# Kernel optimization log

Hardware: AMD Instinct MI355X
Metric: run time of the kernel (lower is better)

## Reference

```python
import jax, jax.numpy as jnp
import numpy as np

# Episode configuration (matches init_kwargs); feature map fixed by module: [64,7,7]
N_WAY, K_SHOT, Q_QUERY, PRJ = 10, 5, 100, 16
DIM, H, W = 64, 7, 7
N_SUP = N_WAY * K_SHOT * PRJ      # 800 support samples
N_QRY = N_WAY * Q_QUERY * PRJ     # 16000 query samples
B = N_SUP + N_QRY                 # 16800
TRIU_I, TRIU_J = np.triu_indices(DIM)  # row-major upper-tri indices, matches torch nonzero order


def setup_inputs() -> dict:
    key = jax.random.key(0)
    k1, k2 = jax.random.split(key)
    feat = jax.random.normal(k1, (B, DIM, H, W), dtype=jnp.float32)
    label = jax.random.randint(k2, (N_QRY,), 0, N_WAY, dtype=jnp.int64)
    # nn.Parameter init: log(1/(2*h*w)) * ones(1,1)
    temp = jnp.log(jnp.ones((1, 1), dtype=jnp.float32) / (2.0 * H * W))
    return {"feat": feat, "temp": temp, "label": label}


def _bdcovpool(x, t):
    # x: [B, dim, h, w] -> Brownian distance covariance matrix [B, dim, dim]
    b, d, h, w = x.shape
    xm = x.reshape(b, d, h * w)
    g = jnp.einsum('bim,bjm->bij', xm, xm)            # x @ x^T, [B,d,d]
    dg = jnp.diagonal(g, axis1=1, axis2=2)            # [B,d]
    # I_M @ (G*I) + (G*I) @ I_M - 2G  ==  diag_j + diag_i - 2G
    dcov = dg[:, None, :] + dg[:, :, None] - 2.0 * g
    dcov = jnp.sqrt(jnp.exp(t) * jnp.clip(dcov, 0.0) + 1e-5)
    # double centering: dcov - rowmean - colmean + totalmean
    rm = jnp.mean(dcov, axis=2, keepdims=True)        # (1/d) dcov @ I_M
    cm = jnp.mean(dcov, axis=1, keepdims=True)        # (1/d) I_M @ dcov
    tm = jnp.mean(dcov, axis=(1, 2), keepdims=True)   # (1/d^2) I_M @ dcov @ I_M
    return dcov - rm - cm + tm


def reference(feat, temp, label):
    v = _bdcovpool(feat, temp)                        # [B, 64, 64]
    tv = v[:, TRIU_I, TRIU_J]                         # Triuvec: [B, 2080]
    support = tv[:N_SUP].reshape(N_WAY, K_SHOT * PRJ, -1).mean(axis=1)  # [n_way, 2080]
    query = tv[N_SUP:]                                # [N_QRY, 2080]
    # negative squared euclidean distance (expanded form of sum((x-y)^2))
    q2 = jnp.sum(query * query, axis=1, keepdims=True)          # [N_QRY,1]
    s2 = jnp.sum(support * support, axis=1)[None, :]             # [1,n_way]
    score = -(q2 + s2 - 2.0 * jnp.einsum('nd,md->nm', query, support))  # [N_QRY, n_way]
    logp = jax.nn.log_softmax(score, axis=-1)
    loss = -jnp.mean(jnp.take_along_axis(logp, label[:, None], axis=1))
    return score, loss
```

## Files before the change

kernel.cpp:

```cpp
#include <hip/hip_runtime.h>
#include <math.h>

#define NWAY   10
#define DIMD   64
#define HWN    49
#define NSUP   800
#define NQRY   16000
#define NTRI   2080
#define FEAT_PER (DIMD*HWN)
#define LDST   68
#define KPAD   72

typedef __attribute__((ext_vector_type(8))) short bf16x8;
typedef __attribute__((ext_vector_type(4))) float f32x4;

struct __align__(16) BDCShared {
    union {
        float dcov[DIMD*LDST];
        unsigned short hl[2*DIMD*KPAD];
    } u;
    float dg[DIMD];
    float rm[DIMD];
    float psum[4*DIMD];
    float red[4*12];
    float tm;
};

__device__ __forceinline__ void k2ij(int k, int& io, int& jo) {
    int ii = (int)floorf((129.0f - sqrtf(16641.0f - 8.0f*(float)k)) * 0.5f);
    int off = ii*(129-ii)/2;
    if (off > k) { --ii; off = ii*(129-ii)/2; }
    else {
        int off2 = (ii+1)*(128-ii)/2;
        if (off2 <= k) { ii += 1; off = off2; }
    }
    io = ii;
    jo = ii + (k - off);
}

__device__ __forceinline__ unsigned short f32_to_bf16_rn(float x) {
    unsigned u = __float_as_uint(x);
    return (unsigned short)((u + 0x7fffu + ((u >> 16) & 1u)) >> 16);
}

__device__ __forceinline__ float bdc_compute(const float* __restrict__ feat,
                                             float et, int sample,
                                             BDCShared& sm) {
    const int tid = threadIdx.x;
    unsigned short* H = sm.u.hl;
    unsigned short* Lp = sm.u.hl + DIMD*KPAD;

    const float4* f4 = (const float4*)(feat + (size_t)sample * FEAT_PER);
    for (int idx = tid; idx < FEAT_PER/4; idx += 256) {
        float4 v = f4[idx];
        int e = idx * 4;
        #pragma unroll
        for (int kk = 0; kk < 4; ++kk) {
            int el = e + kk;
            int d = el / HWN;
            int m = el - d * HWN;
            float x = (&v.x)[kk];
            unsigned short hu = f32_to_bf16_rn(x);
            float hf = __uint_as_float(((unsigned)hu) << 16);
            unsigned short lu = f32_to_bf16_rn(x - hf);
            H[d*KPAD + m]  = hu;
            Lp[d*KPAD + m] = lu;
        }
    }
    for (int p = tid; p < DIMD*16; p += 256) {
        int d = p >> 4, k = 48 + (p & 15);
        if (k >= HWN) { H[d*KPAD + k] = 0; Lp[d*KPAD + k] = 0; }
    }
    __syncthreads();

    const int wv = tid >> 6, lane = tid & 63;
    const int qd = lane >> 4, c15 = lane & 15;
    const int abase = (16*wv + c15)*KPAD + qd*8;
    bf16x8 AH0 = *(const bf16x8*)&H[abase];
    bf16x8 AH1 = *(const bf16x8*)&H[abase + 32];
    bf16x8 AL0 = *(const bf16x8*)&Lp[abase];
    bf16x8 AL1 = *(const bf16x8*)&Lp[abase + 32];

    f32x4 acc[4];
    #pragma unroll
    for (int J = 0; J < 4; ++J) {
        const int bbase = (16*J + c15)*KPAD + qd*8;
        bf16x8 BH0 = *(const bf16x8*)&H[bbase];
        bf16x8 BH1 = *(const bf16x8*)&H[bbase + 32];
        bf16x8 BL0 = *(const bf16x8*)&Lp[bbase];
        bf16x8 BL1 = *(const bf16x8*)&Lp[bbase + 32];
        f32x4 a = {0.f, 0.f, 0.f, 0.f};
        a = __builtin_amdgcn_mfma_f32_16x16x32_bf16(AH0, BH0, a, 0, 0, 0);
        a = __builtin_amdgcn_mfma_f32_16x16x32_bf16(AH1, BH1, a, 0, 0, 0);
        a = __builtin_amdgcn_mfma_f32_16x16x32_bf16(AL0, BH0, a, 0, 0, 0);
        a = __builtin_amdgcn_mfma_f32_16x16x32_bf16(AL1, BH1, a, 0, 0, 0);
        a = __builtin_amdgcn_mfma_f32_16x16x32_bf16(AH0, BL0, a, 0, 0, 0);
        a = __builtin_amdgcn_mfma_f32_16x16x32_bf16(AH1, BL1, a, 0, 0, 0);
        acc[J] = a;
    }

    #pragma unroll
    for (int J = 0; J < 4; ++J) {
        if (J == wv) {
            #pragma unroll
            for (int r = 0; r < 4; ++r)
                if (c15 == 4*qd + r) sm.dg[16*wv + c15] = acc[J][r];
        }
    }
    __syncthreads();

    float* dcov = sm.u.dcov;
    float dgi[4];
    #pragma unroll
    for (int r = 0; r < 4; ++r) dgi[r] = sm.dg[16*wv + 4*qd + r];
    #pragma unroll
    for (int J = 0; J < 4; ++J) {
        int j = 16*J + c15;
        float dgj = sm.dg[j];
        #pragma unroll
        for (int r = 0; r < 4; ++r) {
            int i = 16*wv + 4*qd + r;
            float val = dgi[r] + dgj - 2.0f*acc[J][r];
            dcov[i*LDST + j] = sqrtf(et * fmaxf(val, 0.0f) + 1e-5f);
        }
    }
    __syncthreads();

    {
        int c = tid & 63, q = tid >> 6;
        float s = 0.0f;
        #pragma unroll
        for (int i2 = 0; i2 < 16; ++i2) s += dcov[(q*16 + i2)*LDST + c];
        sm.psum[q*DIMD + c] = s;
    }
    __syncthreads();
    if (tid < DIMD) {
        sm.rm[tid] = (sm.psum[tid] + sm.psum[DIMD+tid] +
                      sm.psum[2*DIMD+tid] + sm.psum[3*DIMD+tid]) * (1.0f/64.0f);
    }
    __syncthreads();
    if (tid < DIMD) {
        float v = sm.rm[tid];
        #pragma unroll
        for (int o = 32; o > 0; o >>= 1) v += __shfl_xor(v, o, 64);
        if (tid == 0) sm.tm = v * (1.0f/64.0f);
    }
    __syncthreads();
    return sm.tm;
}

__global__ void kern_init(float* __restrict__ support,
                          unsigned* __restrict__ table,
                          float* __restrict__ loss_slot) {
    int i = blockIdx.x * 256 + threadIdx.x;
    if (i < NWAY*NTRI) support[i] = 0.0f;
    if (i < NTRI) {
        int ii, jj; k2ij(i, ii, jj);
        table[i] = ((unsigned)(ii*LDST + jj) << 16) | ((unsigned)ii << 8) | (unsigned)jj;
    }
    if (i == 0) loss_slot[0] = 0.0f;
}

__global__ __launch_bounds__(256, 6) void kern_support(const float* __restrict__ feat,
                                                       const float* __restrict__ temp,
                                                       const unsigned* __restrict__ table,
                                                       float* __restrict__ support) {
    __shared__ BDCShared sm;
    float et = __expf(temp[0]);
    int s = blockIdx.x;
    float tm = bdc_compute(feat, et, s, sm);
    float* dst = support + (s / 80) * NTRI;
    for (int k = threadIdx.x; k < NTRI; k += 256) {
        unsigned t = table[k];
        float v = sm.u.dcov[t >> 16] - sm.rm[(t >> 8) & 63] - sm.rm[t & 63] + tm;
        atomicAdd(&dst[k], v * (1.0f/80.0f));
    }
}

__global__ __launch_bounds__(256) void kern_s2(const float* __restrict__ support,
                                               float* __restrict__ s2) {
    __shared__ float red[4];
    int m = blockIdx.x;
    const float* S = support + m * NTRI;
    float acc = 0.0f;
    for (int k = threadIdx.x; k < NTRI; k += 256) acc = fmaf(S[k], S[k], acc);
    int lane = threadIdx.x & 63, wv = threadIdx.x >> 6;
    #pragma unroll
    for (int o = 32; o > 0; o >>= 1) acc += __shfl_xor(acc, o, 64);
    if (lane == 0) red[wv] = acc;
    __syncthreads();
    if (threadIdx.x == 0) s2[m] = red[0] + red[1] + red[2] + red[3];
}

__global__ __launch_bounds__(256, 6) void kern_query(const float* __restrict__ feat,
                                                     const float* __restrict__ temp,
                                                     const unsigned* __restrict__ table,
                                                     const float* __restrict__ support,
                                                     const float* __restrict__ s2,
                                                     float* __restrict__ out) {
    __shared__ BDCShared sm;
    float et = __expf(temp[0]);
    int qn = blockIdx.x;
    float tm = bdc_compute(feat, et, NSUP + qn, sm);

    float qq = 0.0f;
    float cr[NWAY];
    #pragma unroll
    for (int m = 0; m < NWAY; ++m) cr[m] = 0.0f;

    for (int k = threadIdx.x; k < NTRI; k += 256) {
        unsigned t = table[k];
        float v = sm.u.dcov[t >> 16] - sm.rm[(t >> 8) & 63] - sm.rm[t & 63] + tm;
        qq = fmaf(v, v, qq);
        #pragma unroll
        for (int m = 0; m < NWAY; ++m)
            cr[m] = fmaf(v, support[m*NTRI + k], cr[m]);
    }

    int lane = threadIdx.x & 63, wv = threadIdx.x >> 6;
    #pragma unroll
    for (int m = 0; m < NWAY; ++m) {
        float v = cr[m];
        #pragma unroll
        for (int o = 32; o > 0; o >>= 1) v += __shfl_xor(v, o, 64);
        cr[m] = v;
    }
    #pragma unroll
    for (int o = 32; o > 0; o >>= 1) qq += __shfl_xor(qq, o, 64);
    if (lane == 0) {
        #pragma unroll
        for (int m = 0; m < NWAY; ++m) sm.red[wv*12 + m] = cr[m];
        sm.red[wv*12 + 10] = qq;
    }
    __syncthreads();
    if (threadIdx.x < NWAY) {
        int m = threadIdx.x;
        float CR = sm.red[m] + sm.red[12+m] + sm.red[24+m] + sm.red[36+m];
        float QQ = sm.red[10] + sm.red[22] + sm.red[34] + sm.red[46];
        out[(size_t)qn * NWAY + m] = -(QQ + s2[m] - 2.0f*CR);
    }
}

__global__ __launch_bounds__(256) void kern_loss(const float* __restrict__ score,
                                                 const int* __restrict__ label,
                                                 float* __restrict__ loss_out) {
    __shared__ float red[4];
    int n = blockIdx.x * 256 + threadIdx.x;
    float lsum = 0.0f;
    if (n < NQRY) {
        const float* srow = score + (size_t)n * NWAY;
        float s[NWAY];
        float mx = -1e30f;
        #pragma unroll
        for (int m = 0; m < NWAY; ++m) { s[m] = srow[m]; mx = fmaxf(mx, s[m]); }
        float se = 0.0f;
        #pragma unroll
        for (int m = 0; m < NWAY; ++m) se += __expf(s[m] - mx);
        float lse = mx + __logf(se);
        lsum = lse - s[label[n]];
    }
    int lane = threadIdx.x & 63, wv = threadIdx.x >> 6;
    #pragma unroll
    for (int o = 32; o > 0; o >>= 1) lsum += __shfl_xor(lsum, o, 64);
    if (lane == 0) red[wv] = lsum;
    __syncthreads();
    if (threadIdx.x == 0)
        atomicAdd(loss_out, (red[0] + red[1] + red[2] + red[3]) * (1.0f / (float)NQRY));
}

extern "C" void kernel_launch(void* const* d_in, const int* in_sizes, int n_in,
                              void* d_out, int out_size, void* d_ws, size_t ws_size,
                              hipStream_t stream) {
    const float* feat = (const float*)d_in[0];
    const float* temp = (const float*)d_in[1];
    const int*   label = (const int*)d_in[2];
    float* out = (float*)d_out;

    float*    support = (float*)d_ws;
    float*    s2      = support + NWAY*NTRI;
    unsigned* table   = (unsigned*)(s2 + 16);
    float* loss_slot  = out + (size_t)NQRY * NWAY;

    kern_init<<<(NWAY*NTRI + 255)/256, 256, 0, stream>>>(support, table, loss_slot);
    kern_support<<<NSUP, 256, 0, stream>>>(feat, temp, table, support);
    kern_s2<<<NWAY, 256, 0, stream>>>(support, s2);
    kern_query<<<NQRY, 256, 0, stream>>>(feat, temp, table, support, s2, out);
    kern_loss<<<(NQRY + 255)/256, 256, 0, stream>>>(out, label, loss_slot);
}
```

Measured before the change: 382.2 us.

## Restructure BDC staging, fuse row-mean reduction, and transpose support layout

Each thread now loads one 16-element row segment of the feature map and splits it into hi/lo bf16 with the packed v_cvt_pk_bf16_f32 instruction, replacing the per-element divide/modulo and the separate padding loop. Row means and the total mean come from shuffle reductions on the MFMA accumulators, which removes the psum pass and several barriers. dcov is stored transposed to match. Support averaging no longer does global atomics: each support sample writes its triu vector to a workspace, and a separate reduce kernel averages them into a transposed [k][12] layout so the query kernel reads class vectors as three float4s. The cost is a much larger workspace and an extra pass over the 800x2080 intermediate.

Measured after the change: 346.6 us. 1.1x faster.

```diff
diff --git a/kernel.cpp b/kernel.cpp
--- a/kernel.cpp
+++ b/kernel.cpp
@@ -10,6 +10,7 @@
 #define FEAT_PER (DIMD*HWN)
 #define LDST   68
 #define KPAD   72
+#define STP    12
 
 typedef __attribute__((ext_vector_type(8))) short bf16x8;
 typedef __attribute__((ext_vector_type(4))) float f32x4;
@@ -21,9 +22,8 @@
     } u;
     float dg[DIMD];
     float rm[DIMD];
-    float psum[4*DIMD];
+    float w4[4];
     float red[4*12];
-    float tm;
 };
 
 __device__ __forceinline__ void k2ij(int k, int& io, int& jo) {
@@ -38,57 +38,65 @@
     jo = ii + (k - off);
 }
 
-__device__ __forceinline__ unsigned short f32_to_bf16_rn(float x) {
-    unsigned u = __float_as_uint(x);
-    return (unsigned short)((u + 0x7fffu + ((u >> 16) & 1u)) >> 16);
+__device__ __forceinline__ unsigned cvt_pk_bf16(float a, float b) {
+    unsigned r;
+    asm("v_cvt_pk_bf16_f32 %0, %1, %2" : "=v"(r) : "v"(a), "v"(b));
+    return r;
 }
 
 __device__ __forceinline__ float bdc_compute(const float* __restrict__ feat,
                                              float et, int sample,
                                              BDCShared& sm) {
     const int tid = threadIdx.x;
-    unsigned short* H = sm.u.hl;
-    unsigned short* Lp = sm.u.hl + DIMD*KPAD;
-
-    const float4* f4 = (const float4*)(feat + (size_t)sample * FEAT_PER);
-    for (int idx = tid; idx < FEAT_PER/4; idx += 256) {
-        float4 v = f4[idx];
-        int e = idx * 4;
-        #pragma unroll
-        for (int kk = 0; kk < 4; ++kk) {
-            int el = e + kk;
-            int d = el / HWN;
-            int m = el - d * HWN;
-            float x = (&v.x)[kk];
-            unsigned short hu = f32_to_bf16_rn(x);
-            float hf = __uint_as_float(((unsigned)hu) << 16);
-            unsigned short lu = f32_to_bf16_rn(x - hf);
-            H[d*KPAD + m]  = hu;
-            Lp[d*KPAD + m] = lu;
-        }
-    }
-    for (int p = tid; p < DIMD*16; p += 256) {
-        int d = p >> 4, k = 48 + (p & 15);
-        if (k >= HWN) { H[d*KPAD + k] = 0; Lp[d*KPAD + k] = 0; }
+    unsigned short* Hh = sm.u.hl;
+    unsigned short* Lh = sm.u.hl + DIMD*KPAD;
+
+    {
+        const int d = tid & 63, hq = tid >> 6;
+        const float* rowp = feat + (size_t)sample * FEAT_PER + d*HWN + hq*16;
+        float x[16];
+        if (hq < 3) {
+            #pragma unroll
+            for (int i = 0; i < 16; ++i) x[i] = rowp[i];
+        } else {
+            x[0] = rowp[0];
+            #pragma unroll
+            for (int i = 1; i < 16; ++i) x[i] = 0.0f;
+        }
+        unsigned hp[8], lp[8];
+        #pragma unroll
+        for (int i = 0; i < 8; ++i) {
+            unsigned h = cvt_pk_bf16(x[2*i], x[2*i+1]);
+            float h0 = __uint_as_float(h << 16);
+            float h1 = __uint_as_float(h & 0xffff0000u);
+            hp[i] = h;
+            lp[i] = cvt_pk_bf16(x[2*i] - h0, x[2*i+1] - h1);
+        }
+        uint4* hd = (uint4*)&Hh[d*KPAD + hq*16];
+        uint4* ld = (uint4*)&Lh[d*KPAD + hq*16];
+        hd[0] = make_uint4(hp[0], hp[1], hp[2], hp[3]);
+        hd[1] = make_uint4(hp[4], hp[5], hp[6], hp[7]);
+        ld[0] = make_uint4(lp[0], lp[1], lp[2], lp[3]);
+        ld[1] = make_uint4(lp[4], lp[5], lp[6], lp[7]);
     }
     __syncthreads();
 
     const int wv = tid >> 6, lane = tid & 63;
     const int qd = lane >> 4, c15 = lane & 15;
     const int abase = (16*wv + c15)*KPAD + qd*8;
-    bf16x8 AH0 = *(const bf16x8*)&H[abase];
-    bf16x8 AH1 = *(const bf16x8*)&H[abase + 32];
-    bf16x8 AL0 = *(const bf16x8*)&Lp[abase];
-    bf16x8 AL1 = *(const bf16x8*)&Lp[abase + 32];
+    bf16x8 AH0 = *(const bf16x8*)&Hh[abase];
+    bf16x8 AH1 = *(const bf16x8*)&Hh[abase + 32];
+    bf16x8 AL0 = *(const bf16x8*)&Lh[abase];
+    bf16x8 AL1 = *(const bf16x8*)&Lh[abase + 32];
 
     f32x4 acc[4];
     #pragma unroll
     for (int J = 0; J < 4; ++J) {
         const int bbase = (16*J + c15)*KPAD + qd*8;
-        bf16x8 BH0 = *(const bf16x8*)&H[bbase];
-        bf16x8 BH1 = *(const bf16x8*)&H[bbase + 32];
-        bf16x8 BL0 = *(const bf16x8*)&Lp[bbase];
-        bf16x8 BL1 = *(const bf16x8*)&Lp[bbase + 32];
+        bf16x8 BH0 = *(const bf16x8*)&Hh[bbase];
+        bf16x8 BH1 = *(const bf16x8*)&Hh[bbase + 32];
+        bf16x8 BL0 = *(const bf16x8*)&Lh[bbase];
+        bf16x8 BL1 = *(const bf16x8*)&Lh[bbase + 32];
         f32x4 a = {0.f, 0.f, 0.f, 0.f};
         a = __builtin_amdgcn_mfma_f32_16x16x32_bf16(AH0, BH0, a, 0, 0, 0);
         a = __builtin_amdgcn_mfma_f32_16x16x32_bf16(AH1, BH1, a, 0, 0, 0);
@@ -110,92 +118,100 @@
     __syncthreads();
 
     float* dcov = sm.u.dcov;
-    float dgi[4];
-    #pragma unroll
-    for (int r = 0; r < 4; ++r) dgi[r] = sm.dg[16*wv + 4*qd + r];
+    f32x4 dgi = *(const f32x4*)&sm.dg[16*wv + 4*qd];
+    float rs0 = 0.f, rs1 = 0.f, rs2 = 0.f, rs3 = 0.f;
     #pragma unroll
     for (int J = 0; J < 4; ++J) {
-        int j = 16*J + c15;
-        float dgj = sm.dg[j];
+        float dgj = sm.dg[16*J + c15];
+        f32x4 o;
         #pragma unroll
         for (int r = 0; r < 4; ++r) {
-            int i = 16*wv + 4*qd + r;
-            float val = dgi[r] + dgj - 2.0f*acc[J][r];
-            dcov[i*LDST + j] = sqrtf(et * fmaxf(val, 0.0f) + 1e-5f);
-        }
-    }
-    __syncthreads();
-
-    {
-        int c = tid & 63, q = tid >> 6;
-        float s = 0.0f;
-        #pragma unroll
-        for (int i2 = 0; i2 < 16; ++i2) s += dcov[(q*16 + i2)*LDST + c];
-        sm.psum[q*DIMD + c] = s;
-    }
-    __syncthreads();
-    if (tid < DIMD) {
-        sm.rm[tid] = (sm.psum[tid] + sm.psum[DIMD+tid] +
-                      sm.psum[2*DIMD+tid] + sm.psum[3*DIMD+tid]) * (1.0f/64.0f);
-    }
-    __syncthreads();
-    if (tid < DIMD) {
-        float v = sm.rm[tid];
-        #pragma unroll
-        for (int o = 32; o > 0; o >>= 1) v += __shfl_xor(v, o, 64);
-        if (tid == 0) sm.tm = v * (1.0f/64.0f);
-    }
-    __syncthreads();
-    return sm.tm;
-}
-
-__global__ void kern_init(float* __restrict__ support,
-                          unsigned* __restrict__ table,
+            float t2 = fmaf(-2.0f, acc[J][r], dgi[r] + dgj);
+            t2 = fmaxf(t2, 0.0f);
+            o[r] = __builtin_amdgcn_sqrtf(fmaf(et, t2, 1e-5f));
+        }
+        rs0 += o[0]; rs1 += o[1]; rs2 += o[2]; rs3 += o[3];
+        *(f32x4*)&dcov[(16*J + c15)*LDST + 16*wv + 4*qd] = o;
+    }
+    #pragma unroll
+    for (int o = 1; o < 16; o <<= 1) {
+        rs0 += __shfl_xor(rs0, o, 64);
+        rs1 += __shfl_xor(rs1, o, 64);
+        rs2 += __shfl_xor(rs2, o, 64);
+        rs3 += __shfl_xor(rs3, o, 64);
+    }
+    if (c15 == 0) {
+        f32x4 rmv = {rs0*(1.0f/64.0f), rs1*(1.0f/64.0f),
+                     rs2*(1.0f/64.0f), rs3*(1.0f/64.0f)};
+        *(f32x4*)&sm.rm[16*wv + 4*qd] = rmv;
+    }
+    float tt = (rs0 + rs1) + (rs2 + rs3);
+    tt += __shfl_xor(tt, 16, 64);
+    tt += __shfl_xor(tt, 32, 64);
+    if (lane == 0) sm.w4[wv] = tt;
+    __syncthreads();
+    return (sm.w4[0] + sm.w4[1] + sm.w4[2] + sm.w4[3]) * (1.0f/4096.0f);
+}
+
+__global__ void kern_init(unsigned* __restrict__ table,
+                          float* __restrict__ s2,
                           float* __restrict__ loss_slot) {
     int i = blockIdx.x * 256 + threadIdx.x;
-    if (i < NWAY*NTRI) support[i] = 0.0f;
     if (i < NTRI) {
         int ii, jj; k2ij(i, ii, jj);
         table[i] = ((unsigned)(ii*LDST + jj) << 16) | ((unsigned)ii << 8) | (unsigned)jj;
     }
+    if (i < NWAY) s2[i] = 0.0f;
     if (i == 0) loss_slot[0] = 0.0f;
 }
 
 __global__ __launch_bounds__(256, 6) void kern_support(const float* __restrict__ feat,
                                                        const float* __restrict__ temp,
                                                        const unsigned* __restrict__ table,
-                                                       float* __restrict__ support) {
+                                                       float* __restrict__ tvout) {
     __shared__ BDCShared sm;
     float et = __expf(temp[0]);
     int s = blockIdx.x;
     float tm = bdc_compute(feat, et, s, sm);
-    float* dst = support + (s / 80) * NTRI;
+    float* dst = tvout + (size_t)s * NTRI;
     for (int k = threadIdx.x; k < NTRI; k += 256) {
         unsigned t = table[k];
-        float v = sm.u.dcov[t >> 16] - sm.rm[(t >> 8) & 63] - sm.rm[t & 63] + tm;
-        atomicAdd(&dst[k], v * (1.0f/80.0f));
-    }
-}
-
-__global__ __launch_bounds__(256) void kern_s2(const float* __restrict__ support,
-                                               float* __restrict__ s2) {
+        dst[k] = sm.u.dcov[t >> 16] - sm.rm[(t >> 8) & 63] - sm.rm[t & 63] + tm;
+    }
+}
+
+__global__ __launch_bounds__(256) void kern_reduce(const float* __restrict__ tv,
+                                                   float* __restrict__ supT,
+                                                   float* __restrict__ s2) {
     __shared__ float red[4];
-    int m = blockIdx.x;
-    const float* S = support + m * NTRI;
-    float acc = 0.0f;
-    for (int k = threadIdx.x; k < NTRI; k += 256) acc = fmaf(S[k], S[k], acc);
+    int m = blockIdx.x / 9, kc = blockIdx.x % 9;
+    int k = kc*256 + threadIdx.x;
+    float S = 0.0f;
+    if (k < NTRI) {
+        const float* p = tv + (size_t)(80*m) * NTRI + k;
+        float a0 = 0.f, a1 = 0.f, a2 = 0.f, a3 = 0.f;
+        for (int s4 = 0; s4 < 80; s4 += 4) {
+            a0 += p[(size_t)(s4+0)*NTRI];
+            a1 += p[(size_t)(s4+1)*NTRI];
+            a2 += p[(size_t)(s4+2)*NTRI];
+            a3 += p[(size_t)(s4+3)*NTRI];
+        }
+        S = ((a0+a1)+(a2+a3)) * (1.0f/80.0f);
+        supT[k*STP + m] = S;
+    }
+    float ps = S * S;
     int lane = threadIdx.x & 63, wv = threadIdx.x >> 6;
     #pragma unroll
-    for (int o = 32; o > 0; o >>= 1) acc += __shfl_xor(acc, o, 64);
-    if (lane == 0) red[wv] = acc;
-    __syncthreads();
-    if (threadIdx.x == 0) s2[m] = red[0] + red[1] + red[2] + red[3];
+    for (int o = 32; o > 0; o >>= 1) ps += __shfl_xor(ps, o, 64);
+    if (lane == 0) red[wv] = ps;
+    __syncthreads();
+    if (threadIdx.x == 0) atomicAdd(&s2[m], red[0]+red[1]+red[2]+red[3]);
 }
 
 __global__ __launch_bounds__(256, 6) void kern_query(const float* __restrict__ feat,
                                                      const float* __restrict__ temp,
                                                      const unsigned* __restrict__ table,
-                                                     const float* __restrict__ support,
+                                                     const float* __restrict__ supT,
                                                      const float* __restrict__ s2,
                                                      float* __restrict__ out) {
     __shared__ BDCShared sm;
@@ -212,9 +228,18 @@
         unsigned t = table[k];
         float v = sm.u.dcov[t >> 16] - sm.rm[(t >> 8) & 63] - sm.rm[t & 63] + tm;
         qq = fmaf(v, v, qq);
-        #pragma unroll
-        for (int m = 0; m < NWAY; ++m)
-            cr[m] = fmaf(v, support[m*NTRI + k], cr[m]);
+        const float4* sp = (const float4*)(supT + (size_t)k * STP);
+        float4 sa = sp[0], sb = sp[1], sc = sp[2];
+        cr[0] = fmaf(v, sa.x, cr[0]);
+        cr[1] = fmaf(v, sa.y, cr[1]);
+        cr[2] = fmaf(v, sa.z, cr[2]);
+        cr[3] = fmaf(v, sa.w, cr[3]);
+        cr[4] = fmaf(v, sb.x, cr[4]);
+        cr[5] = fmaf(v, sb.y, cr[5]);
+        cr[6] = fmaf(v, sb.z, cr[6]);
+        cr[7] = fmaf(v, sb.w, cr[7]);
+        cr[8] = fmaf(v, sc.x, cr[8]);
+        cr[9] = fmaf(v, sc.y, cr[9]);
     }
 
     int lane = threadIdx.x & 63, wv = threadIdx.x >> 6;
@@ -276,14 +301,15 @@
     const int*   label = (const int*)d_in[2];
     float* out = (float*)d_out;
 
-    float*    support = (float*)d_ws;
-    float*    s2      = support + NWAY*NTRI;
-    unsigned* table   = (unsigned*)(s2 + 16);
-    float* loss_slot  = out + (size_t)NQRY * NWAY;
-
-    kern_init<<<(NWAY*NTRI + 255)/256, 256, 0, stream>>>(support, table, loss_slot);
-    kern_support<<<NSUP, 256, 0, stream>>>(feat, temp, table, support);
-    kern_s2<<<NWAY, 256, 0, stream>>>(support, s2);
-    kern_query<<<NQRY, 256, 0, stream>>>(feat, temp, table, support, s2, out);
+    float*    tv    = (float*)d_ws;
+    float*    supT  = tv + (size_t)NSUP * NTRI;
+    float*    s2    = supT + NTRI*STP;
+    unsigned* table = (unsigned*)(s2 + 16);
+    float* loss_slot = out + (size_t)NQRY * NWAY;
+
+    kern_init<<<(NTRI + 255)/256, 256, 0, stream>>>(table, s2, loss_slot);
+    kern_support<<<NSUP, 256, 0, stream>>>(feat, temp, table, tv);
+    kern_reduce<<<NWAY*9, 256, 0, stream>>>(tv, supT, s2);
+    kern_query<<<NQRY, 256, 0, stream>>>(feat, temp, table, supT, s2, out);
     kern_loss<<<(NQRY + 255)/256, 256, 0, stream>>>(out, label, loss_slot);
 }
```
